# Kernel optimization log

Hardware: AMD Instinct MI355X
Metric: run time of the kernel (lower is better)

Reference implementation:

```python
import jax, jax.numpy as jnp
import numpy as np

H = 1024  # hidden_size
NH = 16   # num_heads
HD = H // NH  # head_dim

def setup_inputs() -> dict:
    key = jax.random.key(0)
    ks = jax.random.split(key, 7)
    s = 1.0 / np.sqrt(H)
    return {
        "hidden": jax.random.normal(ks[0], (2, 2048, H), dtype=jnp.float32),
        "Wq": jax.random.normal(ks[1], (H, H), dtype=jnp.float32) * s,
        "bq": jnp.zeros((H,), dtype=jnp.float32),
        "Wk": jax.random.normal(ks[2], (H, H), dtype=jnp.float32) * s,
        "bk": jnp.zeros((H,), dtype=jnp.float32),
        "Wv": jax.random.normal(ks[3], (H, H), dtype=jnp.float32) * s,
        "bv": jnp.zeros((H,), dtype=jnp.float32),
    }

def _split_heads(x):
    # [B, S, H] -> [B, NH, S, HD]
    b, s, _ = x.shape
    return x.reshape(b, s, NH, HD).transpose(0, 2, 1, 3)

def reference(hidden, Wq, bq, Wk, bk, Wv, bv):
    q = _split_heads(hidden @ Wq.T + bq)
    k = _split_heads(hidden @ Wk.T + bk)
    v = _split_heads(hidden @ Wv.T + bv)
    scores = jnp.einsum("bhqd,bhkd->bhqk", q, k) / jnp.sqrt(jnp.float32(HD))
    probs = jax.nn.softmax(scores, axis=-1)  # dropout is identity in eval
    ctx = jnp.einsum("bhqk,bhkd->bhqd", probs, v)
    b, _, s, _ = ctx.shape
    return ctx.transpose(0, 2, 1, 3).reshape(b, s, NH * HD)
```

## Files before the change

kernel.cpp:

```cpp
#include <hip/hip_runtime.h>


typedef __attribute__((ext_vector_type(8))) short bf16x8;
typedef __attribute__((ext_vector_type(4))) float f32x4;

#define L2E 1.44269504088896340736f

__device__ __forceinline__ unsigned short f2bf(float x) {
  union { float f; unsigned int u; } a; a.f = x;
  unsigned int r = (a.u + 0x7fffu + ((a.u >> 16) & 1u)) >> 16;
  return (unsigned short)r;
}
__device__ __forceinline__ unsigned int fbits(float x) {
  union { float f; unsigned int u; } a; a.f = x; return a.u;
}

__device__ __forceinline__ bf16x8 pack_bf16x8(float p0, float p1, float p2, float p3,
                                              float p4, float p5, float p6, float p7) {
#if defined(__AMDGCN__) && __has_builtin(__builtin_amdgcn_cvt_pk_bf16_f32)
  typedef __attribute__((ext_vector_type(2))) __bf16 bf16x2_t;
  union { bf16x2_t h[4]; bf16x8 v; } pk;
  pk.h[0] = __builtin_amdgcn_cvt_pk_bf16_f32(p0, p1);
  pk.h[1] = __builtin_amdgcn_cvt_pk_bf16_f32(p2, p3);
  pk.h[2] = __builtin_amdgcn_cvt_pk_bf16_f32(p4, p5);
  pk.h[3] = __builtin_amdgcn_cvt_pk_bf16_f32(p6, p7);
  return pk.v;
#else
  unsigned u0 = fbits(p0) + 0x8000u, u1 = fbits(p1) + 0x8000u;
  unsigned u2 = fbits(p2) + 0x8000u, u3 = fbits(p3) + 0x8000u;
  unsigned u4 = fbits(p4) + 0x8000u, u5 = fbits(p5) + 0x8000u;
  unsigned u6 = fbits(p6) + 0x8000u, u7 = fbits(p7) + 0x8000u;
  union { unsigned u[4]; bf16x8 v; } pk;
  pk.u[0] = __builtin_amdgcn_perm(u1, u0, 0x07060302u);
  pk.u[1] = __builtin_amdgcn_perm(u3, u2, 0x07060302u);
  pk.u[2] = __builtin_amdgcn_perm(u5, u4, 0x07060302u);
  pk.u[3] = __builtin_amdgcn_perm(u7, u6, 0x07060302u);
  return pk.v;
#endif
}

__device__ __forceinline__ void gl_lds16(const unsigned short* g, unsigned short* l) {
  __builtin_amdgcn_global_load_lds(
      (const __attribute__((address_space(1))) void*)g,
      (__attribute__((address_space(3))) void*)l, 16, 0, 0);
}

__global__ __launch_bounds__(256) void convert_all(
    const float* __restrict__ hidden, const float* __restrict__ Wq,
    const float* __restrict__ Wk, const float* __restrict__ Wv,
    unsigned short* __restrict__ Xb, unsigned short* __restrict__ Wqb,
    unsigned short* __restrict__ Wkb, unsigned short* __restrict__ Wvb) {
  int i = blockIdx.x * 256 + threadIdx.x;
  const float* src; unsigned short* dst; int off;
  if (i < 1048576)      { src = hidden; dst = Xb;  off = i; }
  else if (i < 1310720) { src = Wq;     dst = Wqb; off = i - 1048576; }
  else if (i < 1572864) { src = Wk;     dst = Wkb; off = i - 1310720; }
  else                  { src = Wv;     dst = Wvb; off = i - 1572864; }
  float4 v = ((const float4*)src)[off];
  ushort4 o;
  o.x = f2bf(v.x); o.y = f2bf(v.y); o.z = f2bf(v.z); o.w = f2bf(v.w);
  ((ushort4*)dst)[off] = o;
}

__global__ __launch_bounds__(256) void qkv_gemm(
    const unsigned short* __restrict__ Xb,
    const unsigned short* __restrict__ Wqb, const unsigned short* __restrict__ Wkb,
    const unsigned short* __restrict__ Wvb,
    const float* __restrict__ bq, const float* __restrict__ bk,
    const float* __restrict__ bv,
    unsigned short* __restrict__ Qh, unsigned short* __restrict__ Kh,
    unsigned short* __restrict__ Vh) {
  const int id  = blockIdx.x;
  const int xcd = id & 7;
  const int j   = id >> 3;
  const int tok = xcd * 4 + (j & 3);
  const int k2  = j >> 2;
  const int ft  = k2 & 7;
  const int z   = k2 >> 3;

  const unsigned short* Ap; const unsigned short* Bp;
  const float* bias; unsigned short* Out; int m0, n0;
  if (z == 2) {
    Ap = Wvb; Bp = Xb; bias = bv; Out = Vh;
    m0 = ft * 128; n0 = tok * 128;
  } else {
    Ap = Xb; Bp = (z == 0) ? Wqb : Wkb; bias = (z == 0) ? bq : bk;
    Out = (z == 0) ? Qh : Kh;
    m0 = tok * 128; n0 = ft * 128;
  }
  const float oscale = (z == 0) ? (0.125f * L2E) : 1.0f;

  __shared__ unsigned short As[128 * 64];
  __shared__ unsigned short Bs[128 * 64];

  const int tid  = threadIdx.x;
  const int lane = tid & 63;
  const int w    = tid >> 6;
  const int wm   = w >> 1, wn = w & 1;
  const int quad = lane >> 4;
  const int r    = lane & 15;

  f32x4 acc[4][4];
#pragma unroll
  for (int a = 0; a < 4; a++)
#pragma unroll
    for (int c = 0; c < 4; c++) acc[a][c] = (f32x4){0.f, 0.f, 0.f, 0.f};

  for (int k0 = 0; k0 < 1024; k0 += 64) {
    __syncthreads();
#pragma unroll
    for (int i = 0; i < 4; i++) {
      int t   = w * 4 + i;
      int blk = t * 64 + lane;
      int row = blk >> 3;
      int c   = (blk & 7) ^ (row & 7);
      gl_lds16(Ap + (size_t)(m0 + row) * 1024 + k0 + c * 8, &As[t * 512]);
      gl_lds16(Bp + (size_t)(n0 + row) * 1024 + k0 + c * 8, &Bs[t * 512]);
    }
    __syncthreads();

    bf16x8 af[4][2], bfv[4][2];
#pragma unroll
    for (int mi = 0; mi < 4; mi++)
#pragma unroll
      for (int ks = 0; ks < 2; ks++) {
        int row = wm * 64 + mi * 16 + r;
        int bc  = (ks * 4 + quad) ^ (row & 7);
        af[mi][ks] = *(const bf16x8*)&As[row * 64 + bc * 8];
      }
#pragma unroll
    for (int ni = 0; ni < 4; ni++)
#pragma unroll
      for (int ks = 0; ks < 2; ks++) {
        int row = wn * 64 + ni * 16 + r;
        int bc  = (ks * 4 + quad) ^ (row & 7);
        bfv[ni][ks] = *(const bf16x8*)&Bs[row * 64 + bc * 8];
      }
#pragma unroll
    for (int mi = 0; mi < 4; mi++)
#pragma unroll
      for (int ni = 0; ni < 4; ni++) {
        acc[mi][ni] = __builtin_amdgcn_mfma_f32_16x16x32_bf16(af[mi][0], bfv[ni][0], acc[mi][ni], 0, 0, 0);
        acc[mi][ni] = __builtin_amdgcn_mfma_f32_16x16x32_bf16(af[mi][1], bfv[ni][1], acc[mi][ni], 0, 0, 0);
      }
  }

  if (z == 2) {
#pragma unroll
    for (int mi = 0; mi < 4; mi++)
#pragma unroll
      for (int e = 0; e < 4; e++) {
        int m = m0 + wm * 64 + mi * 16 + quad * 4 + e;
        float bm = bias[m];
#pragma unroll
        for (int ni = 0; ni < 4; ni++) {
          int n = n0 + wn * 64 + ni * 16 + r;
          int bb = n >> 11, s = n & 2047;
          int hh = m >> 6,  d = m & 63;
          float v = acc[mi][ni][e] + bm;
          Out[((size_t)(bb * 16 + hh) * 64 + d) * 2048 + s] = f2bf(v);
        }
      }
  } else {
    float biasv[4];
#pragma unroll
    for (int ni = 0; ni < 4; ni++) biasv[ni] = bias[n0 + wn * 64 + ni * 16 + r];
#pragma unroll
    for (int mi = 0; mi < 4; mi++)
#pragma unroll
      for (int ni = 0; ni < 4; ni++)
#pragma unroll
        for (int e = 0; e < 4; e++) {
          int m = m0 + wm * 64 + mi * 16 + quad * 4 + e;
          int n = n0 + wn * 64 + ni * 16 + r;
          int bb = m >> 11, s = m & 2047;
          int hh = n >> 6,  d = n & 63;
          float v = (acc[mi][ni][e] + biasv[ni]) * oscale;
          Out[((size_t)(bb * 16 + hh) * 2048 + s) * 64 + d] = f2bf(v);
        }
  }
}

__device__ __forceinline__ void attn_tile(
    const unsigned short* SMbase, int boff,
    const int kfo[2][4], const int vfo[2][4],
    const bf16x8 aq0[2], const bf16x8 aq1[2],
    const bf16x8 ones8, f32x4 lacc[2], f32x4 acc[2][4]) {
  const f32x4 zero4 = (f32x4){0.f, 0.f, 0.f, 0.f};
#pragma unroll
  for (int ncp = 0; ncp < 2; ncp++) {
    bf16x8 kA0 = *(const bf16x8*)&SMbase[kfo[ncp][0] + boff];
    bf16x8 kA1 = *(const bf16x8*)&SMbase[kfo[ncp][1] + boff];
    bf16x8 kB0 = *(const bf16x8*)&SMbase[kfo[ncp][2] + boff];
    bf16x8 kB1 = *(const bf16x8*)&SMbase[kfo[ncp][3] + boff];

    bf16x8 ap8[2];
#pragma unroll
    for (int jq = 0; jq < 2; jq++) {
      f32x4 tA  = __builtin_amdgcn_mfma_f32_16x16x32_bf16(kA1, aq1[jq], zero4, 0, 0, 0);
      f32x4 sTA = __builtin_amdgcn_mfma_f32_16x16x32_bf16(kA0, aq0[jq], tA, 0, 0, 0);
      f32x4 tB  = __builtin_amdgcn_mfma_f32_16x16x32_bf16(kB1, aq1[jq], zero4, 0, 0, 0);
      f32x4 sTB = __builtin_amdgcn_mfma_f32_16x16x32_bf16(kB0, aq0[jq], tB, 0, 0, 0);

      float pa0 = __builtin_exp2f(sTA[0]);
      float pa1 = __builtin_exp2f(sTA[1]);
      float pa2 = __builtin_exp2f(sTA[2]);
      float pa3 = __builtin_exp2f(sTA[3]);
      float pb0 = __builtin_exp2f(sTB[0]);
      float pb1 = __builtin_exp2f(sTB[1]);
      float pb2 = __builtin_exp2f(sTB[2]);
      float pb3 = __builtin_exp2f(sTB[3]);
      ap8[jq] = pack_bf16x8(pa0, pa1, pa2, pa3, pb0, pb1, pb2, pb3);
    }

    bf16x8 vf[4];
#pragma unroll
    for (int dc = 0; dc < 4; dc++)
      vf[dc] = *(const bf16x8*)&SMbase[vfo[ncp][dc] + boff];

#pragma unroll
    for (int jq = 0; jq < 2; jq++) {
      lacc[jq] = __builtin_amdgcn_mfma_f32_16x16x32_bf16(ap8[jq], ones8, lacc[jq], 0, 0, 0);
#pragma unroll
      for (int dc = 0; dc < 4; dc++)
        acc[jq][dc] = __builtin_amdgcn_mfma_f32_16x16x32_bf16(ap8[jq], vf[dc], acc[jq][dc], 0, 0, 0);
    }
  }
}

__global__ __launch_bounds__(512, 4) void attn(
    const unsigned short* __restrict__ Qh, const unsigned short* __restrict__ Kh,
    const unsigned short* __restrict__ Vh, float* __restrict__ Out) {
  const int h = blockIdx.y, b = blockIdx.z;
  const int bh = b * 16 + h;
  const int q0 = blockIdx.x * 128;
  const unsigned short* Qp  = Qh + (size_t)bh * 2048 * 64;
  const unsigned short* Kp  = Kh + (size_t)bh * 2048 * 64;
  const unsigned short* VTp = Vh + (size_t)bh * 64 * 2048;

  __shared__ __align__(16) char SMRAW[65536];
  unsigned short* SMbase = (unsigned short*)SMRAW;

  const int tid  = threadIdx.x;
  const int lane = tid & 63;
  const int w8   = tid >> 6;
  const int half = w8 >> 2;
  const int w    = w8 & 3;
  const int ltid = tid & 255;
  const int quad = lane >> 4;
  const int r    = lane & 15;

  const int kvbase = half * 1024;
  const int gK = half * 8192;
  const int gV = gK + 4096;

  const int blk0 = ltid, blk1 = 256 + ltid;
  const int row0 = blk0 >> 3, cs0 = blk0 & 7;
  const int row1 = blk1 >> 3, cs1 = blk1 & 7;
  const int sk0 = ((row0 >> 3) + 2 * (row0 & 7)) & 7;
  const int sk1 = ((row1 >> 3) + 2 * (row1 & 7)) & 7;
  const unsigned short* gK0 = Kp + (size_t)(kvbase + row0) * 64 + ((cs0 ^ sk0) * 8);
  const unsigned short* gK1 = Kp + (size_t)(kvbase + row1) * 64 + ((cs1 ^ sk1) * 8);
  const unsigned short* gV0 = VTp + (size_t)row0 * 2048 + kvbase + (((cs0 + 5 * row0) & 7) * 8);
  const unsigned short* gV1 = VTp + (size_t)row1 * 2048 + kvbase + (((cs1 + 5 * row1) & 7) * 8);
  const int dKo0 = gK + blk0 * 8, dKo1 = gK + blk1 * 8;
  const int dVo0 = gV + blk0 * 8, dVo1 = gV + blk1 * 8;

#define STAGE(BOFF)                                        \
  do {                                                     \
    gl_lds16(gK0, &SMbase[dKo0 + (BOFF)]);                 \
    gl_lds16(gK1, &SMbase[dKo1 + (BOFF)]);                 \
    gl_lds16(gV0, &SMbase[dVo0 + (BOFF)]);                 \
    gl_lds16(gV1, &SMbase[dVo1 + (BOFF)]);                 \
    gK0 += 64 * 64; gK1 += 64 * 64; gV0 += 64; gV1 += 64;  \
  } while (0)

  STAGE(0);

  const int prow = ((r >> 2) << 3) + (r & 3);
  int kfo[2][4], vfo[2][4];
#pragma unroll
  for (int ncp = 0; ncp < 2; ncp++) {
    const int rowA = ncp * 32 + prow;
    const int rowB = rowA + 4;
    const int sA = ((rowA >> 3) + 2 * (rowA & 7)) & 7;
    const int sB = ((rowB >> 3) + 2 * (rowB & 7)) & 7;
    kfo[ncp][0] = gK + rowA * 64 + ((quad ^ sA) * 8);
    kfo[ncp][1] = gK + rowA * 64 + (((4 + quad) ^ sA) * 8);
    kfo[ncp][2] = gK + rowB * 64 + ((quad ^ sB) * 8);
    kfo[ncp][3] = gK + rowB * 64 + (((4 + quad) ^ sB) * 8);
#pragma unroll
    for (int dc = 0; dc < 4; dc++) {
      const int vrow = dc * 16 + r;
      const int slot = (4 * ncp + quad + 3 * vrow) & 7;
      vfo[ncp][dc] = gV + vrow * 64 + slot * 8;
    }
  }

  const unsigned short* qbase = Qp + (size_t)(q0 + w * 32 + r) * 64 + quad * 8;
  bf16x8 aq0[2], aq1[2];
  aq0[0] = *(const bf16x8*)(qbase);
  aq1[0] = *(const bf16x8*)(qbase + 32);
  aq0[1] = *(const bf16x8*)(qbase + 16 * 64);
  aq1[1] = *(const bf16x8*)(qbase + 16 * 64 + 32);

  f32x4 lacc[2];
  lacc[0] = (f32x4){0.f, 0.f, 0.f, 0.f};
  lacc[1] = (f32x4){0.f, 0.f, 0.f, 0.f};
  f32x4 acc[2][4];
#pragma unroll
  for (int jq = 0; jq < 2; jq++)
#pragma unroll
    for (int dc = 0; dc < 4; dc++) acc[jq][dc] = (f32x4){0.f, 0.f, 0.f, 0.f};

  union { unsigned u[4]; bf16x8 v; } ou;
  ou.u[0] = 0x3F803F80u; ou.u[1] = 0x3F803F80u;
  ou.u[2] = 0x3F803F80u; ou.u[3] = 0x3F803F80u;
  const bf16x8 ones8 = ou.v;

  __syncthreads();

#pragma unroll 1
  for (int it = 0; it < 8; ++it) {
    STAGE(16384);
    __builtin_amdgcn_s_setprio(1);
    attn_tile(SMbase, 0, kfo, vfo, aq0, aq1, ones8, lacc, acc);
    __builtin_amdgcn_s_setprio(0);
    __syncthreads();

    if (it < 7) STAGE(0);
    __builtin_amdgcn_s_setprio(1);
    attn_tile(SMbase, 16384, kfo, vfo, aq0, aq1, ones8, lacc, acc);
    __builtin_amdgcn_s_setprio(0);
    __syncthreads();
  }
#undef STAGE

  float* Abuf = (float*)SMRAW;
  float* Lbuf = Abuf + 128 * 65;
  if (half == 1) {
#pragma unroll
    for (int jq = 0; jq < 2; jq++)
#pragma unroll
      for (int e = 0; e < 4; e++) {
        int q = w * 32 + jq * 16 + quad * 4 + e;
#pragma unroll
        for (int dc = 0; dc < 4; dc++)
          Abuf[q * 65 + dc * 16 + r] = acc[jq][dc][e];
        if (r == 0) Lbuf[q] = lacc[jq][e];
      }
  }
  __syncthreads();
  if (half == 0) {
#pragma unroll
    for (int jq = 0; jq < 2; jq++)
#pragma unroll
      for (int e = 0; e < 4; e++) {
        int q = w * 32 + jq * 16 + quad * 4 + e;
        float l = lacc[jq][e] + Lbuf[q];
        float inv = 1.f / l;
        int s = q0 + q;
#pragma unroll
        for (int dc = 0; dc < 4; dc++) {
          int d = dc * 16 + r;
          float v = acc[jq][dc][e] + Abuf[q * 65 + d];
          Out[(size_t)(b * 2048 + s) * 1024 + h * 64 + d] = v * inv;
        }
      }
  }
}

extern "C" void kernel_launch(void* const* d_in, const int* in_sizes, int n_in,
                              void* d_out, int out_size, void* d_ws, size_t ws_size,
                              hipStream_t stream) {
  const float* hidden = (const float*)d_in[0];
  const float* Wq = (const float*)d_in[1];
  const float* bq = (const float*)d_in[2];
  const float* Wk = (const float*)d_in[3];
  const float* bk = (const float*)d_in[4];
  const float* Wv = (const float*)d_in[5];
  const float* bv = (const float*)d_in[6];
  float* out = (float*)d_out;

  char* ws = (char*)d_ws;
  unsigned short* Qhp = (unsigned short*)(ws + 0);
  unsigned short* Khp = (unsigned short*)(ws + 8388608);
  unsigned short* Vhp = (unsigned short*)(ws + 16777216);
  unsigned short* Xb  = (unsigned short*)(ws + 25165824);
  unsigned short* Wqb = (unsigned short*)(ws + 33554432);
  unsigned short* Wkb = (unsigned short*)(ws + 35651584);
  unsigned short* Wvb = (unsigned short*)(ws + 37748736);

  convert_all<<<7168, 256, 0, stream>>>(hidden, Wq, Wk, Wv, Xb, Wqb, Wkb, Wvb);
  qkv_gemm<<<768, 256, 0, stream>>>(Xb, Wqb, Wkb, Wvb, bq, bk, bv,
                                    Qhp, Khp, Vhp);
  attn<<<dim3(16, 16, 2), 512, 0, stream>>>(Qhp, Khp, Vhp, out);
}
```

Before: 177.4 us.

## Double attention query tile per block to 256 rows for K/V reuse

Result: no change. 179.4 us (+1.1%).

```diff
diff --git a/kernel.cpp b/kernel.cpp
--- a/kernel.cpp
+++ b/kernel.cpp
@@ -184,8 +184,8 @@
 __device__ __forceinline__ void attn_tile(
     const unsigned short* SMbase, int boff,
     const int kfo[2][4], const int vfo[2][4],
-    const bf16x8 aq0[2], const bf16x8 aq1[2],
-    const bf16x8 ones8, f32x4 lacc[2], f32x4 acc[2][4]) {
+    const bf16x8 aq0[4], const bf16x8 aq1[4],
+    const bf16x8 ones8, f32x4 lacc[4], f32x4 acc[4][4]) {
   const f32x4 zero4 = (f32x4){0.f, 0.f, 0.f, 0.f};
 #pragma unroll
   for (int ncp = 0; ncp < 2; ncp++) {
@@ -194,9 +194,9 @@
     bf16x8 kB0 = *(const bf16x8*)&SMbase[kfo[ncp][2] + boff];
     bf16x8 kB1 = *(const bf16x8*)&SMbase[kfo[ncp][3] + boff];
 
-    bf16x8 ap8[2];
-#pragma unroll
-    for (int jq = 0; jq < 2; jq++) {
+    bf16x8 ap8[4];
+#pragma unroll
+    for (int jq = 0; jq < 4; jq++) {
       f32x4 tA  = __builtin_amdgcn_mfma_f32_16x16x32_bf16(kA1, aq1[jq], zero4, 0, 0, 0);
       f32x4 sTA = __builtin_amdgcn_mfma_f32_16x16x32_bf16(kA0, aq0[jq], tA, 0, 0, 0);
       f32x4 tB  = __builtin_amdgcn_mfma_f32_16x16x32_bf16(kB1, aq1[jq], zero4, 0, 0, 0);
@@ -219,7 +219,7 @@
       vf[dc] = *(const bf16x8*)&SMbase[vfo[ncp][dc] + boff];
 
 #pragma unroll
-    for (int jq = 0; jq < 2; jq++) {
+    for (int jq = 0; jq < 4; jq++) {
       lacc[jq] = __builtin_amdgcn_mfma_f32_16x16x32_bf16(ap8[jq], ones8, lacc[jq], 0, 0, 0);
 #pragma unroll
       for (int dc = 0; dc < 4; dc++)
@@ -228,12 +228,12 @@
   }
 }
 
-__global__ __launch_bounds__(512, 4) void attn(
+__global__ __launch_bounds__(512, 2) void attn(
     const unsigned short* __restrict__ Qh, const unsigned short* __restrict__ Kh,
     const unsigned short* __restrict__ Vh, float* __restrict__ Out) {
   const int h = blockIdx.y, b = blockIdx.z;
   const int bh = b * 16 + h;
-  const int q0 = blockIdx.x * 128;
+  const int q0 = blockIdx.x * 256;
   const unsigned short* Qp  = Qh + (size_t)bh * 2048 * 64;
   const unsigned short* Kp  = Kh + (size_t)bh * 2048 * 64;
   const unsigned short* VTp = Vh + (size_t)bh * 64 * 2048;
@@ -297,21 +297,22 @@
     }
   }
 
-  const unsigned short* qbase = Qp + (size_t)(q0 + w * 32 + r) * 64 + quad * 8;
-  bf16x8 aq0[2], aq1[2];
-  aq0[0] = *(const bf16x8*)(qbase);
-  aq1[0] = *(const bf16x8*)(qbase + 32);
-  aq0[1] = *(const bf16x8*)(qbase + 16 * 64);
-  aq1[1] = *(const bf16x8*)(qbase + 16 * 64 + 32);
-
-  f32x4 lacc[2];
-  lacc[0] = (f32x4){0.f, 0.f, 0.f, 0.f};
-  lacc[1] = (f32x4){0.f, 0.f, 0.f, 0.f};
-  f32x4 acc[2][4];
-#pragma unroll
-  for (int jq = 0; jq < 2; jq++)
+  const unsigned short* qbase = Qp + (size_t)(q0 + w * 64 + r) * 64 + quad * 8;
+  bf16x8 aq0[4], aq1[4];
+#pragma unroll
+  for (int jq = 0; jq < 4; jq++) {
+    aq0[jq] = *(const bf16x8*)(qbase + jq * 16 * 64);
+    aq1[jq] = *(const bf16x8*)(qbase + jq * 16 * 64 + 32);
+  }
+
+  f32x4 lacc[4];
+  f32x4 acc[4][4];
+#pragma unroll
+  for (int jq = 0; jq < 4; jq++) {
+    lacc[jq] = (f32x4){0.f, 0.f, 0.f, 0.f};
 #pragma unroll
     for (int dc = 0; dc < 4; dc++) acc[jq][dc] = (f32x4){0.f, 0.f, 0.f, 0.f};
+  }
 
   union { unsigned u[4]; bf16x8 v; } ou;
   ou.u[0] = 0x3F803F80u; ou.u[1] = 0x3F803F80u;
@@ -338,35 +339,43 @@
 
   float* Abuf = (float*)SMRAW;
   float* Lbuf = Abuf + 128 * 65;
-  if (half == 1) {
-#pragma unroll
-    for (int jq = 0; jq < 2; jq++)
-#pragma unroll
-      for (int e = 0; e < 4; e++) {
-        int q = w * 32 + jq * 16 + quad * 4 + e;
-#pragma unroll
-        for (int dc = 0; dc < 4; dc++)
-          Abuf[q * 65 + dc * 16 + r] = acc[jq][dc][e];
-        if (r == 0) Lbuf[q] = lacc[jq][e];
-      }
-  }
-  __syncthreads();
-  if (half == 0) {
-#pragma unroll
-    for (int jq = 0; jq < 2; jq++)
-#pragma unroll
-      for (int e = 0; e < 4; e++) {
-        int q = w * 32 + jq * 16 + quad * 4 + e;
-        float l = lacc[jq][e] + Lbuf[q];
-        float inv = 1.f / l;
-        int s = q0 + q;
-#pragma unroll
-        for (int dc = 0; dc < 4; dc++) {
-          int d = dc * 16 + r;
-          float v = acc[jq][dc][e] + Abuf[q * 65 + d];
-          Out[(size_t)(b * 2048 + s) * 1024 + h * 64 + d] = v * inv;
+#pragma unroll
+  for (int round = 0; round < 2; ++round) {
+    __syncthreads();
+    if (half == 1) {
+#pragma unroll
+      for (int jq2 = 0; jq2 < 2; jq2++) {
+        int jq = round * 2 + jq2;
+#pragma unroll
+        for (int e = 0; e < 4; e++) {
+          int qc = w * 32 + jq2 * 16 + quad * 4 + e;
+#pragma unroll
+          for (int dc = 0; dc < 4; dc++)
+            Abuf[qc * 65 + dc * 16 + r] = acc[jq][dc][e];
+          if (r == 0) Lbuf[qc] = lacc[jq][e];
         }
       }
+    }
+    __syncthreads();
+    if (half == 0) {
+#pragma unroll
+      for (int jq2 = 0; jq2 < 2; jq2++) {
+        int jq = round * 2 + jq2;
+#pragma unroll
+        for (int e = 0; e < 4; e++) {
+          int qc = w * 32 + jq2 * 16 + quad * 4 + e;
+          float l = lacc[jq][e] + Lbuf[qc];
+          float inv = 1.f / l;
+          int s = q0 + w * 64 + jq * 16 + quad * 4 + e;
+#pragma unroll
+          for (int dc = 0; dc < 4; dc++) {
+            int d = dc * 16 + r;
+            float v = acc[jq][dc][e] + Abuf[qc * 65 + d];
+            Out[(size_t)(b * 2048 + s) * 1024 + h * 64 + d] = v * inv;
+          }
+        }
+      }
+    }
   }
 }
 
@@ -394,5 +403,5 @@
   convert_all<<<7168, 256, 0, stream>>>(hidden, Wq, Wk, Wv, Xb, Wqb, Wkb, Wvb);
   qkv_gemm<<<768, 256, 0, stream>>>(Xb, Wqb, Wkb, Wvb, bq, bk, bv,
                                     Qhp, Khp, Vhp);
-  attn<<<dim3(16, 16, 2), 512, 0, stream>>>(Qhp, Khp, Vhp, out);
-}
+  attn<<<dim3(8, 16, 2), 512, 0, stream>>>(Qhp, Khp, Vhp, out);
+}
```
